# Kernel tuning notes

Hardware: AMD Instinct MI355X
Metric: run time of the kernel (lower is better)

## Reference

```python
import jax, jax.numpy as jnp
import numpy as np

N_QUERY, N_BACKGND, DIM = 2048, 8192, 32


def setup_inputs() -> dict:
    key = jax.random.key(0)
    k0, k1, k2, k3 = jax.random.split(key, 4)
    x_backgnd = jax.random.normal(k0, (N_BACKGND, DIM), dtype=jnp.float32)
    y_backgnd = jax.random.normal(k1, (N_BACKGND,), dtype=jnp.float32)
    x_query = jax.random.normal(k2, (N_QUERY, DIM), dtype=jnp.float32)
    r = jax.random.uniform(k3, (N_QUERY, N_BACKGND), dtype=jnp.float32)
    sigma = jnp.array([0.1], dtype=jnp.float32)      # nn.Parameter init_sigma
    r_scale = jnp.array([3.0], dtype=jnp.float32)    # nn.Parameter init_r_scale
    w = jnp.ones((DIM,), dtype=jnp.float32)          # trainable weights matrix
    return {"x_backgnd": x_backgnd, "y_backgnd": y_backgnd, "x_query": x_query,
            "r": r, "sigma": sigma, "r_scale": r_scale, "w": w}


def reference(x_backgnd, y_backgnd, x_query, r, sigma, r_scale, w):
    # weighted Euclidean distance: ||(xq - xb) * w|| via the expansion trick,
    # avoiding the (n_query, n_backgnd, dim) difference tensor.
    xq = x_query * w           # (nq, d)
    xb = x_backgnd * w         # (nb, d)
    q2 = jnp.sum(xq * xq, axis=1, keepdims=True)        # (nq, 1)
    b2 = jnp.sum(xb * xb, axis=1)                        # (nb,)
    d2 = q2 + b2[None, :] - 2.0 * (xq @ xb.T)            # (nq, nb)
    dists = jnp.sqrt(jnp.maximum(d2, 0.0))
    # exp kernel with relationship bias, normalize, weighted sum
    k_vals = jnp.exp(-dists / sigma + r_scale * r)       # sigma, r_scale broadcast (1,)
    k_sum = jnp.sum(k_vals, axis=1, keepdims=True) + 1e-8
    weights = k_vals / k_sum
    y_pred = weights @ y_backgnd                          # (nq,)
    return y_pred
```

## Files before the change

kernel.cpp:

```cpp
#include <hip/hip_runtime.h>
#include <math.h>

#define NQ 2048
#define NB 8192
#define DIM 32

#define LOG2E 1.44269504088896340736f

typedef _Float16 half8 __attribute__((ext_vector_type(8)));
typedef float    f32x4 __attribute__((ext_vector_type(4)));

#define WS_ACC 0
#define WS_Q2  16448
#define WS_B2  24640
#define WS_XQH 57408
#define WS_XBH 188480

__global__ __launch_bounds__(256) void relnw_pre(
    const float* __restrict__ xq, const float* __restrict__ xb,
    const float* __restrict__ w,
    _Float16* __restrict__ XQh, _Float16* __restrict__ XBh,
    float* __restrict__ q2, float* __restrict__ b2,
    float* __restrict__ acc)
{
    const int tid = threadIdx.x;
    const int gi  = blockIdx.x * 256 + tid;
    if (gi < 2 * NQ) acc[gi] = 0.f;

    const int row = blockIdx.x * 64 + (tid >> 2);
    const int p   = tid & 3;
    if (row >= NQ + NB) return;

    const float* src; _Float16* dst; float* s2; float scale;
    if (row < NQ) { src = xq + (size_t)row * DIM;
                    dst = XQh + (size_t)row * DIM; s2 = q2 + row; scale = 1.f; }
    else          { int j = row - NQ;
                    src = xb + (size_t)j * DIM;
                    dst = XBh + (size_t)j * DIM;   s2 = b2 + j;   scale = -2.f; }

    const float4 xa  = ((const float4*)src)[p * 2];
    const float4 xbv = ((const float4*)src)[p * 2 + 1];
    const float4 wa  = ((const float4*)w)[p * 2];
    const float4 wb  = ((const float4*)w)[p * 2 + 1];
    const float xs[8]  = {xa.x, xa.y, xa.z, xa.w, xbv.x, xbv.y, xbv.z, xbv.w};
    const float ws_[8] = {wa.x, wa.y, wa.z, wa.w, wb.x, wb.y, wb.z, wb.w};

    half8 h;
    float s = 0.f;
#pragma unroll
    for (int c = 0; c < 8; ++c) {
        float t = xs[c] * ws_[c];
        _Float16 hh = (_Float16)t;
        float th = (float)hh;
        s = fmaf(th, th, s);
        h[c] = (_Float16)(th * scale);
    }
    *(half8*)(dst + p * 8) = h;

    s += __shfl_xor(s, 1, 64);
    s += __shfl_xor(s, 2, 64);
    if (p == 0) *s2 = s;
}

#define BT_PER_WAVE 16
#define BG_PER_WAVE (BT_PER_WAVE * 16)

__global__ __launch_bounds__(256, 2) void relnw_main(
    const _Float16* __restrict__ XQh,
    const _Float16* __restrict__ XBh,
    const float* __restrict__ q2,
    const float* __restrict__ b2,
    const float* __restrict__ yb,
    const float* __restrict__ r,
    const float* __restrict__ sigma,
    const float* __restrict__ rscale,
    float* __restrict__ acc)
{
    const int tid  = threadIdx.x;
    const int lane = tid & 63;
    const int wid  = tid >> 6;
    const int m    = lane & 15;
    const int quad = lane >> 4;

    const int q0     = blockIdx.y * 16;
    const int bstart = (blockIdx.x * 4 + wid) * BG_PER_WAVE;

    const float c1 = -LOG2E / sigma[0];
    const float c2 =  LOG2E * rscale[0];

    const half8 qfrag = *(const half8*)(XQh + (size_t)(q0 + m) * DIM + quad * 8);
    const float q2s   = q2[q0 + m];

    const _Float16* xbp = XBh + (size_t)(bstart + m) * DIM + quad * 8;
    const float*    rp  = r  + (size_t)(q0 + m) * NB + bstart + quad * 4;
    const float*    ybp = yb + bstart + quad * 4;
    const float*    b2p = b2 + bstart + quad * 4;

    float sk = 0.f, sky = 0.f;

    f32x4 rrb[8];
    half8 af[3];
    f32x4 yv[3], bb[3];

#pragma unroll
    for (int i = 0; i < 2; ++i) {
        af[i] = *(const half8*)(xbp + (size_t)i * 16 * DIM);
        yv[i] = *(const f32x4*)(ybp + i * 16);
        bb[i] = *(const f32x4*)(b2p + i * 16);
    }
#pragma unroll
    for (int i = 0; i < 8; ++i)
        rrb[i] = *(const f32x4*)(rp + i * 16);

#pragma unroll
    for (int it = 0; it < 16; ++it) {
        const int cs = it % 3;
        const int ns = (it + 2) % 3;
        if (it + 2 < 16) {
            af[ns] = *(const half8*)(xbp + (size_t)(it + 2) * 16 * DIM);
            yv[ns] = *(const f32x4*)(ybp + (it + 2) * 16);
            bb[ns] = *(const f32x4*)(b2p + (it + 2) * 16);
        }

        f32x4 cin;
#pragma unroll
        for (int g = 0; g < 4; ++g) cin[g] = q2s + bb[cs][g];

        f32x4 d2v = __builtin_amdgcn_mfma_f32_16x16x32_f16(
            af[cs], qfrag, cin, 0, 0, 0);

        const int rs = it & 7;
#pragma unroll
        for (int g = 0; g < 4; ++g) {
            float d2   = fmaxf(d2v[g], 0.f);
            float dist = __builtin_amdgcn_sqrtf(d2);
            float e    = fmaf(dist, c1, rrb[rs][g] * c2);
            float k    = __builtin_amdgcn_exp2f(e);
            sk += k;
            sky = fmaf(k, yv[cs][g], sky);
        }

        if (it + 8 < 16)
            rrb[rs] = *(const f32x4*)(rp + (it + 8) * 16);
    }

    sk  += __shfl_xor(sk, 16, 64);
    sk  += __shfl_xor(sk, 32, 64);
    sky += __shfl_xor(sky, 16, 64);
    sky += __shfl_xor(sky, 32, 64);
    if (lane < 16) {
        atomicAdd(acc + (q0 + m),      sk);
        atomicAdd(acc + NQ + (q0 + m), sky);
    }
}

__global__ __launch_bounds__(256) void relnw_finalize(
    const float* __restrict__ acc, float* __restrict__ out)
{
    int q = blockIdx.x * 256 + threadIdx.x;
    if (q < NQ)
        out[q] = acc[NQ + q] / (acc[q] + 1e-8f);
}

extern "C" void kernel_launch(void* const* d_in, const int* in_sizes, int n_in,
                              void* d_out, int out_size, void* d_ws, size_t ws_size,
                              hipStream_t stream) {
    const float* xb     = (const float*)d_in[0];
    const float* yb     = (const float*)d_in[1];
    const float* xq     = (const float*)d_in[2];
    const float* r      = (const float*)d_in[3];
    const float* sigma  = (const float*)d_in[4];
    const float* rscale = (const float*)d_in[5];
    const float* w      = (const float*)d_in[6];
    float* out = (float*)d_out;

    char* ws = (char*)d_ws;
    float*    acc = (float*)(ws + WS_ACC);
    float*    q2  = (float*)(ws + WS_Q2);
    float*    b2  = (float*)(ws + WS_B2);
    _Float16* XQh = (_Float16*)(ws + WS_XQH);
    _Float16* XBh = (_Float16*)(ws + WS_XBH);

    relnw_pre<<<(NQ + NB) / 64, 256, 0, stream>>>(xq, xb, w, XQh, XBh, q2, b2, acc);

    dim3 grid(NB / (4 * BG_PER_WAVE), NQ / 16);
    relnw_main<<<grid, 256, 0, stream>>>(XQh, XBh, q2, b2, yb, r, sigma, rscale, acc);

    relnw_finalize<<<(NQ + 255) / 256, 256, 0, stream>>>(acc, out);
}
```

Before: 117.9 us.

## Stage r, b2, yb tiles into LDS via global_load_lds with swizzle

Replaces per-lane register-pipelined global loads of the r matrix, b2 and yb with direct global-to-LDS loads. Each wave copies its r tile (16 rows x 128 columns per half) into LDS using full-row contiguous 512-byte segments and an XOR swizzle to avoid bank conflicts. It then reads the fragments back from LDS in MFMA layout. The aim is coalesced wide loads of r instead of strided 16-byte per-row accesses. In exchange it adds explicit vmcnt(0) waits that serialize load and compute between the two halves, and 40KB of LDS per block that may limit occupancy.

```diff
diff --git a/kernel.cpp b/kernel.cpp
--- a/kernel.cpp
+++ b/kernel.cpp
@@ -64,6 +64,18 @@
 
 #define BT_PER_WAVE 16
 #define BG_PER_WAVE (BT_PER_WAVE * 16)
+
+#define GLDS(GSRC, LDST)                                                    \
+  __builtin_amdgcn_global_load_lds(                                         \
+      (const __attribute__((address_space(1))) void*)(GSRC),                \
+      (__attribute__((address_space(3))) void*)(LDST), 16, 0, 0)
+
+#define WAIT_VM0                                                            \
+  { asm volatile("s_waitcnt vmcnt(0)" ::: "memory");                        \
+    __builtin_amdgcn_sched_barrier(0); }
+#define WAIT_LGKM0                                                          \
+  { asm volatile("s_waitcnt lgkmcnt(0)" ::: "memory");                      \
+    __builtin_amdgcn_sched_barrier(0); }
 
 __global__ __launch_bounds__(256, 2) void relnw_main(
     const _Float16* __restrict__ XQh,
@@ -76,6 +88,8 @@
     const float* __restrict__ rscale,
     float* __restrict__ acc)
 {
+    __shared__ char lds[4 * 8192 + 4 * 1024 + 4 * 1024];
+
     const int tid  = threadIdx.x;
     const int lane = tid & 63;
     const int wid  = tid >> 6;
@@ -85,63 +99,80 @@
     const int q0     = blockIdx.y * 16;
     const int bstart = (blockIdx.x * 4 + wid) * BG_PER_WAVE;
 
+    char*  waveR = lds + wid * 8192;
+    float* b2l   = (float*)(lds + 32768 + wid * 1024);
+    float* ybl   = (float*)(lds + 36864 + wid * 1024);
+
     const float c1 = -LOG2E / sigma[0];
     const float c2 =  LOG2E * rscale[0];
 
     const half8 qfrag = *(const half8*)(XQh + (size_t)(q0 + m) * DIM + quad * 8);
     const float q2s   = q2[q0 + m];
-
-    const _Float16* xbp = XBh + (size_t)(bstart + m) * DIM + quad * 8;
-    const float*    rp  = r  + (size_t)(q0 + m) * NB + bstart + quad * 4;
-    const float*    ybp = yb + bstart + quad * 4;
-    const float*    b2p = b2 + bstart + quad * 4;
+    const int   swz   = (m & 7) << 4;
+
+    GLDS((const char*)(b2 + bstart) + lane * 16, b2l);
+    GLDS((const char*)(yb + bstart) + lane * 16, ybl);
+
+    const int jj = lane >> 5;
+    const int cc = lane & 31;
+    const char* rsrc[8];
+#pragma unroll
+    for (int j = 0; j < 8; ++j) {
+        const int rw = 2 * j + jj;
+        rsrc[j] = (const char*)(r + (size_t)(q0 + rw) * NB + bstart)
+                  + ((cc * 16) ^ ((rw & 7) << 4));
+    }
+
+#pragma unroll
+    for (int j = 0; j < 8; ++j) GLDS(rsrc[j], waveR + j * 1024);
+
+    half8 af[8];
+#pragma unroll
+    for (int i = 0; i < 8; ++i)
+        af[i] = *(const half8*)(XBh + (size_t)(bstart + i * 16 + m) * DIM + quad * 8);
 
     float sk = 0.f, sky = 0.f;
 
-    f32x4 rrb[8];
-    half8 af[3];
-    f32x4 yv[3], bb[3];
-
-#pragma unroll
-    for (int i = 0; i < 2; ++i) {
-        af[i] = *(const half8*)(xbp + (size_t)i * 16 * DIM);
-        yv[i] = *(const f32x4*)(ybp + i * 16);
-        bb[i] = *(const f32x4*)(b2p + i * 16);
-    }
-#pragma unroll
-    for (int i = 0; i < 8; ++i)
-        rrb[i] = *(const f32x4*)(rp + i * 16);
-
-#pragma unroll
-    for (int it = 0; it < 16; ++it) {
-        const int cs = it % 3;
-        const int ns = (it + 2) % 3;
-        if (it + 2 < 16) {
-            af[ns] = *(const half8*)(xbp + (size_t)(it + 2) * 16 * DIM);
-            yv[ns] = *(const f32x4*)(ybp + (it + 2) * 16);
-            bb[ns] = *(const f32x4*)(b2p + (it + 2) * 16);
+    WAIT_VM0
+
+#pragma unroll
+    for (int h = 0; h < 2; ++h) {
+        if (h == 1) {
+#pragma unroll
+            for (int i = 0; i < 8; ++i)
+                af[i] = *(const half8*)(XBh +
+                        (size_t)(bstart + 128 + i * 16 + m) * DIM + quad * 8);
+            WAIT_LGKM0
+#pragma unroll
+            for (int j = 0; j < 8; ++j) GLDS(rsrc[j] + 512, waveR + j * 1024);
+            WAIT_VM0
         }
 
-        f32x4 cin;
-#pragma unroll
-        for (int g = 0; g < 4; ++g) cin[g] = q2s + bb[cs][g];
-
-        f32x4 d2v = __builtin_amdgcn_mfma_f32_16x16x32_f16(
-            af[cs], qfrag, cin, 0, 0, 0);
-
-        const int rs = it & 7;
-#pragma unroll
-        for (int g = 0; g < 4; ++g) {
-            float d2   = fmaxf(d2v[g], 0.f);
-            float dist = __builtin_amdgcn_sqrtf(d2);
-            float e    = fmaf(dist, c1, rrb[rs][g] * c2);
-            float k    = __builtin_amdgcn_exp2f(e);
-            sk += k;
-            sky = fmaf(k, yv[cs][g], sky);
+#pragma unroll
+        for (int it = 0; it < 8; ++it) {
+            const int co = h * 128 + it * 16 + quad * 4;
+            const f32x4 bb = *(const f32x4*)(b2l + co);
+            const f32x4 yv = *(const f32x4*)(ybl + co);
+            const f32x4 rr = *(const f32x4*)(waveR + m * 512 +
+                                 ((it * 64 + quad * 16) ^ swz));
+
+            f32x4 cin;
+#pragma unroll
+            for (int g = 0; g < 4; ++g) cin[g] = q2s + bb[g];
+
+            const f32x4 d2v = __builtin_amdgcn_mfma_f32_16x16x32_f16(
+                af[it], qfrag, cin, 0, 0, 0);
+
+#pragma unroll
+            for (int g = 0; g < 4; ++g) {
+                float d2   = fmaxf(d2v[g], 0.f);
+                float dist = __builtin_amdgcn_sqrtf(d2);
+                float e    = fmaf(dist, c1, rr[g] * c2);
+                float k    = __builtin_amdgcn_exp2f(e);
+                sk += k;
+                sky = fmaf(k, yv[g], sky);
+            }
         }
-
-        if (it + 8 < 16)
-            rrb[rs] = *(const f32x4*)(rp + (it + 8) * 16);
     }
 
     sk  += __shfl_xor(sk, 16, 64);
```

Measured after the change: 109.2 us. 7.4% less time.

## Stage r tile into LDS via global_load_lds and compute query fp16 in-kernel

Applied to the files above, without the earlier changes.

The main kernel now copies the whole 16x1024 r tile, plus matching b2 and yb slices, into LDS with direct global-to-LDS loads. It waits for all of them at a single barrier, then reads from LDS in the compute loop, replacing the per-wave register prefetch ring. Query fp16 conversion and q2 are computed inside the main kernel, so the pre-kernel only converts the background rows. The intent is wide coalesced streaming of r. In exchange the loads are no longer overlapped with compute, since everything is waited on up front, and the 72KB of LDS per block may limit occupancy.

```diff
diff --git a/kernel.cpp b/kernel.cpp
--- a/kernel.cpp
+++ b/kernel.cpp
@@ -11,16 +11,12 @@
 typedef float    f32x4 __attribute__((ext_vector_type(4)));
 
 #define WS_ACC 0
-#define WS_Q2  16448
 #define WS_B2  24640
-#define WS_XQH 57408
 #define WS_XBH 188480
 
 __global__ __launch_bounds__(256) void relnw_pre(
-    const float* __restrict__ xq, const float* __restrict__ xb,
-    const float* __restrict__ w,
-    _Float16* __restrict__ XQh, _Float16* __restrict__ XBh,
-    float* __restrict__ q2, float* __restrict__ b2,
+    const float* __restrict__ xb, const float* __restrict__ w,
+    _Float16* __restrict__ XBh, float* __restrict__ b2,
     float* __restrict__ acc)
 {
     const int tid = threadIdx.x;
@@ -29,14 +25,10 @@
 
     const int row = blockIdx.x * 64 + (tid >> 2);
     const int p   = tid & 3;
-    if (row >= NQ + NB) return;
-
-    const float* src; _Float16* dst; float* s2; float scale;
-    if (row < NQ) { src = xq + (size_t)row * DIM;
-                    dst = XQh + (size_t)row * DIM; s2 = q2 + row; scale = 1.f; }
-    else          { int j = row - NQ;
-                    src = xb + (size_t)j * DIM;
-                    dst = XBh + (size_t)j * DIM;   s2 = b2 + j;   scale = -2.f; }
+    if (row >= NB) return;
+
+    const float* src = xb + (size_t)row * DIM;
+    _Float16*    dst = XBh + (size_t)row * DIM;
 
     const float4 xa  = ((const float4*)src)[p * 2];
     const float4 xbv = ((const float4*)src)[p * 2 + 1];
@@ -53,95 +45,118 @@
         _Float16 hh = (_Float16)t;
         float th = (float)hh;
         s = fmaf(th, th, s);
-        h[c] = (_Float16)(th * scale);
+        h[c] = (_Float16)(th * -2.f);
     }
     *(half8*)(dst + p * 8) = h;
 
     s += __shfl_xor(s, 1, 64);
     s += __shfl_xor(s, 2, 64);
-    if (p == 0) *s2 = s;
-}
-
-#define BT_PER_WAVE 16
-#define BG_PER_WAVE (BT_PER_WAVE * 16)
+    if (p == 0) b2[row] = s;
+}
+
+#define GLDS(GSRC, LDST)                                                    \
+  __builtin_amdgcn_global_load_lds(                                         \
+      (const __attribute__((address_space(1))) void*)(GSRC),                \
+      (__attribute__((address_space(3))) void*)(LDST), 16, 0, 0)
+
+#define SBAR __builtin_amdgcn_sched_barrier(0)
 
 __global__ __launch_bounds__(256, 2) void relnw_main(
-    const _Float16* __restrict__ XQh,
     const _Float16* __restrict__ XBh,
-    const float* __restrict__ q2,
     const float* __restrict__ b2,
     const float* __restrict__ yb,
+    const float* __restrict__ xq,
+    const float* __restrict__ w,
     const float* __restrict__ r,
     const float* __restrict__ sigma,
     const float* __restrict__ rscale,
     float* __restrict__ acc)
 {
+    __shared__ char lds[16 * 4096 + 4096 + 4096];
+
     const int tid  = threadIdx.x;
     const int lane = tid & 63;
     const int wid  = tid >> 6;
     const int m    = lane & 15;
     const int quad = lane >> 4;
 
-    const int q0     = blockIdx.y * 16;
-    const int bstart = (blockIdx.x * 4 + wid) * BG_PER_WAVE;
+    const int q0    = blockIdx.y * 16;
+    const int bcol0 = blockIdx.x * 1024;
+
+    float* b2l = (float*)(lds + 65536);
+    float* ybl = (float*)(lds + 69632);
 
     const float c1 = -LOG2E / sigma[0];
     const float c2 =  LOG2E * rscale[0];
 
-    const half8 qfrag = *(const half8*)(XQh + (size_t)(q0 + m) * DIM + quad * 8);
-    const float q2s   = q2[q0 + m];
-
-    const _Float16* xbp = XBh + (size_t)(bstart + m) * DIM + quad * 8;
-    const float*    rp  = r  + (size_t)(q0 + m) * NB + bstart + quad * 4;
-    const float*    ybp = yb + bstart + quad * 4;
-    const float*    b2p = b2 + bstart + quad * 4;
+    const float4 qa = ((const float4*)(xq + (size_t)(q0 + m) * DIM))[quad * 2];
+    const float4 qb = ((const float4*)(xq + (size_t)(q0 + m) * DIM))[quad * 2 + 1];
+    const float4 wa = ((const float4*)w)[quad * 2];
+    const float4 wb = ((const float4*)w)[quad * 2 + 1];
+
+#pragma unroll
+    for (int j = 0; j < 4; ++j) {
+        const int rw = wid * 4 + j;
+        const char* rbase = (const char*)(r + (size_t)(q0 + rw) * NB + bcol0)
+                            + lane * 16;
+#pragma unroll
+        for (int ck = 0; ck < 4; ++ck)
+            GLDS(rbase + ck * 1024, lds + rw * 4096 + ck * 1024);
+    }
+    GLDS((const char*)(b2 + bcol0) + wid * 1024 + lane * 16,
+         (char*)b2l + wid * 1024);
+    GLDS((const char*)(yb + bcol0) + wid * 1024 + lane * 16,
+         (char*)ybl + wid * 1024);
+
+    const float xs[8]  = {qa.x, qa.y, qa.z, qa.w, qb.x, qb.y, qb.z, qb.w};
+    const float ws_[8] = {wa.x, wa.y, wa.z, wa.w, wb.x, wb.y, wb.z, wb.w};
+    half8 qfrag;
+    float s = 0.f;
+#pragma unroll
+    for (int c = 0; c < 8; ++c) {
+        float t = xs[c] * ws_[c];
+        _Float16 hh = (_Float16)t;
+        float th = (float)hh;
+        s = fmaf(th, th, s);
+        qfrag[c] = hh;
+    }
+    s += __shfl_xor(s, 16, 64);
+    s += __shfl_xor(s, 32, 64);
+    const float q2s = s;
+
+    SBAR;
+    asm volatile("s_waitcnt vmcnt(0)" ::: "memory");
+    SBAR;
+    __builtin_amdgcn_s_barrier();
 
     float sk = 0.f, sky = 0.f;
-
-    f32x4 rrb[8];
-    half8 af[3];
-    f32x4 yv[3], bb[3];
-
-#pragma unroll
-    for (int i = 0; i < 2; ++i) {
-        af[i] = *(const half8*)(xbp + (size_t)i * 16 * DIM);
-        yv[i] = *(const f32x4*)(ybp + i * 16);
-        bb[i] = *(const f32x4*)(b2p + i * 16);
-    }
-#pragma unroll
-    for (int i = 0; i < 8; ++i)
-        rrb[i] = *(const f32x4*)(rp + i * 16);
-
 #pragma unroll
     for (int it = 0; it < 16; ++it) {
-        const int cs = it % 3;
-        const int ns = (it + 2) % 3;
-        if (it + 2 < 16) {
-            af[ns] = *(const half8*)(xbp + (size_t)(it + 2) * 16 * DIM);
-            yv[ns] = *(const f32x4*)(ybp + (it + 2) * 16);
-            bb[ns] = *(const f32x4*)(b2p + (it + 2) * 16);
-        }
+        const int col0 = bcol0 + wid * 256 + it * 16;
+        const half8 af = *(const half8*)(XBh +
+                         (size_t)(col0 + m) * DIM + quad * 8);
+        const int co = wid * 256 + it * 16 + quad * 4;
+        const f32x4 bb = *(const f32x4*)(b2l + co);
+        const f32x4 yv = *(const f32x4*)(ybl + co);
+        const f32x4 rr = *(const f32x4*)(lds + m * 4096 +
+                             wid * 1024 + it * 64 + quad * 16);
 
         f32x4 cin;
 #pragma unroll
-        for (int g = 0; g < 4; ++g) cin[g] = q2s + bb[cs][g];
-
-        f32x4 d2v = __builtin_amdgcn_mfma_f32_16x16x32_f16(
-            af[cs], qfrag, cin, 0, 0, 0);
-
-        const int rs = it & 7;
+        for (int g = 0; g < 4; ++g) cin[g] = q2s + bb[g];
+
+        const f32x4 d2v = __builtin_amdgcn_mfma_f32_16x16x32_f16(
+            af, qfrag, cin, 0, 0, 0);
+
 #pragma unroll
         for (int g = 0; g < 4; ++g) {
             float d2   = fmaxf(d2v[g], 0.f);
             float dist = __builtin_amdgcn_sqrtf(d2);
-            float e    = fmaf(dist, c1, rrb[rs][g] * c2);
+            float e    = fmaf(dist, c1, rr[g] * c2);
             float k    = __builtin_amdgcn_exp2f(e);
             sk += k;
-            sky = fmaf(k, yv[cs][g], sky);
+            sky = fmaf(k, yv[g], sky);
         }
-
-        if (it + 8 < 16)
-            rrb[rs] = *(const f32x4*)(rp + (it + 8) * 16);
     }
 
     sk  += __shfl_xor(sk, 16, 64);
@@ -176,15 +191,14 @@
 
     char* ws = (char*)d_ws;
     float*    acc = (float*)(ws + WS_ACC);
-    float*    q2  = (float*)(ws + WS_Q2);
     float*    b2  = (float*)(ws + WS_B2);
-    _Float16* XQh = (_Float16*)(ws + WS_XQH);
     _Float16* XBh = (_Float16*)(ws + WS_XBH);
 
-    relnw_pre<<<(NQ + NB) / 64, 256, 0, stream>>>(xq, xb, w, XQh, XBh, q2, b2, acc);
-
-    dim3 grid(NB / (4 * BG_PER_WAVE), NQ / 16);
-    relnw_main<<<grid, 256, 0, stream>>>(XQh, XBh, q2, b2, yb, r, sigma, rscale, acc);
+    relnw_pre<<<NB / 64, 256, 0, stream>>>(xb, w, XBh, b2, acc);
+
+    dim3 grid(NB / 1024, NQ / 16);
+    relnw_main<<<grid, 256, 0, stream>>>(XBh, b2, yb, xq, w, r,
+                                         sigma, rscale, acc);
 
     relnw_finalize<<<(NQ + 255) / 256, 256, 0, stream>>>(acc, out);
 }
```

After: 112.3 us. 1.05x faster.
